# Kernel tuning notes

Hardware: AMD Instinct MI355X
Metric: run time of the kernel (lower is better)

## Reference

```python
import jax, jax.numpy as jnp
import numpy as np

N = 100000   # nodes
E = 400000   # edges (before self-loops)
G = 4000     # graphs in batch
F_IN = 32    # node_embedding
HID = 128    # hidden_channels
H = 3        # heads (hard-coded in module)
W3 = H * HID # 384, post-concat width
NC = 10      # num_classes
NL = 4       # num_layers
NEG_SLOPE = 0.2


def _lin(key, fan_in, fan_out):
    return jax.random.normal(key, (fan_in, fan_out), jnp.float32) * (1.0 / np.sqrt(fan_in))


def setup_inputs() -> dict:
    key = jax.random.key(0)
    ks = iter(jax.random.split(key, 40))
    x = jax.random.normal(next(ks), (N, F_IN), jnp.float32)
    edge_index = jax.random.randint(next(ks), (2, E), 0, N, dtype=jnp.int32)
    batch = jnp.sort(jax.random.randint(next(ks), (N,), 0, G, dtype=jnp.int32))
    inp = dict(x=x, edge_index=edge_index, batch=batch)
    # MLP stem
    inp['lin1_w'] = _lin(next(ks), F_IN, 2 * HID); inp['lin1_b'] = jnp.zeros((2 * HID,), jnp.float32)
    inp['lin2_w'] = _lin(next(ks), 2 * HID, HID);  inp['lin2_b'] = jnp.zeros((HID,), jnp.float32)
    # conv1: GATConv(HID -> HID, heads=3)
    inp['w0'] = _lin(next(ks), HID, W3)
    inp['as0'] = jax.random.normal(next(ks), (H, HID), jnp.float32) * 0.1
    inp['ad0'] = jax.random.normal(next(ks), (H, HID), jnp.float32) * 0.1
    inp['b0'] = jnp.zeros((W3,), jnp.float32)
    # remaining NL-1 convs: GATConv(W3 -> HID, heads=3), stacked
    inp['wl'] = jnp.stack([_lin(next(ks), W3, W3) for _ in range(NL - 1)])
    inp['asl'] = jax.random.normal(next(ks), (NL - 1, H, HID), jnp.float32) * 0.1
    inp['adl'] = jax.random.normal(next(ks), (NL - 1, H, HID), jnp.float32) * 0.1
    inp['bl'] = jnp.zeros((NL - 1, W3), jnp.float32)
    # batch norms (NL total, all width W3)
    inp['gamma'] = jnp.ones((NL, W3), jnp.float32)
    inp['beta'] = jnp.zeros((NL, W3), jnp.float32)
    # head
    inp['lin3_w'] = _lin(next(ks), W3, HID); inp['lin3_b'] = jnp.zeros((HID,), jnp.float32)
    inp['lin4_w'] = _lin(next(ks), HID, NC); inp['lin4_b'] = jnp.zeros((NC,), jnp.float32)
    return inp


def _gat(x, W, a_src, a_dst, bias, src, dst):
    # PyG GATConv, concat heads. x: [N, Fin]
    h = (x @ W).reshape(N, H, HID)                       # [N, H, C]
    es = jnp.einsum('nhc,hc->nh', h, a_src)              # [N, H]
    ed = jnp.einsum('nhc,hc->nh', h, a_dst)
    e = jax.nn.leaky_relu(es[src] + ed[dst], NEG_SLOPE)  # [Etot, H]
    m = jax.ops.segment_max(e, dst, num_segments=N)      # segment softmax over incoming edges
    p = jnp.exp(e - m[dst])
    s = jax.ops.segment_sum(p, dst, num_segments=N)
    alpha = p / s[dst]                                   # every node has a self-loop -> s>0
    out = jax.ops.segment_sum(alpha[:, :, None] * h[src], dst, num_segments=N)
    return out.reshape(N, W3) + bias


def _bn(x, g, b):
    mu = x.mean(0)
    var = x.var(0)
    return (x - mu) * jax.lax.rsqrt(var + 1e-5) * g + b


def reference(x, edge_index, batch, lin1_w, lin1_b, lin2_w, lin2_b,
              w0, as0, ad0, b0, wl, asl, adl, bl, gamma, beta,
              lin3_w, lin3_b, lin4_w, lin4_b):
    loop = jnp.arange(N, dtype=edge_index.dtype)
    src = jnp.concatenate([edge_index[0], loop])  # add_self_loops=True (PyG default)
    dst = jnp.concatenate([edge_index[1], loop])
    h = jax.nn.relu(x @ lin1_w + lin1_b)
    h = jax.nn.relu(h @ lin2_w + lin2_b)
    h = _gat(h, w0, as0, ad0, b0, src, dst)
    h = _bn(h, gamma[0], beta[0])
    for i in range(NL - 1):
        h = _gat(h, wl[i], asl[i], adl[i], bl[i], src, dst)
        h = _bn(h, gamma[i + 1], beta[i + 1])
    # global mean pool over graphs
    sums = jax.ops.segment_sum(h, batch, num_segments=G)
    cnt = jax.ops.segment_sum(jnp.ones((N,), h.dtype), batch, num_segments=G)
    g = sums / jnp.maximum(cnt, 1.0)[:, None]
    g = jax.nn.relu(g @ lin3_w + lin3_b)
    logits = g @ lin4_w + lin4_b
    return jax.nn.log_softmax(logits, axis=-1)
```

## Files before the change

### kernel.cpp

```cpp
#include <hip/hip_runtime.h>

#define NN      100000
#define NN2     100096
#define NE      400000
#define ETOT    500000
#define NG      4000
#define W3D     384
#define HIDD    128
#define NCLS    10
#define NSLICE  256

typedef unsigned short u16;
typedef unsigned int   u32;
typedef unsigned long long u64;
typedef __attribute__((ext_vector_type(8))) short short8;
typedef __attribute__((ext_vector_type(4))) float f32x4;

static __device__ __forceinline__ float bf2f(u16 u) {
  return __uint_as_float(((u32)u) << 16);
}
static __device__ __forceinline__ float bflo(u32 u) {
  return __uint_as_float(u << 16);
}
static __device__ __forceinline__ float bfhi(u32 u) {
  return __uint_as_float(u & 0xffff0000u);
}
static __device__ __forceinline__ u16 f2b(float f) {
  u32 u = __float_as_uint(f);
  u32 r = (u + 0x7fffu + ((u >> 16) & 1u)) >> 16;
  return (u16)r;
}

static __device__ __forceinline__ void llds16(const u16* g, u16* l) {
  __builtin_amdgcn_global_load_lds(
      (const __attribute__((address_space(1))) void*)(u64)(const void*)g,
      (__attribute__((address_space(3))) void*)(u64)(void*)l, 16, 0, 0);
}

#define WAITV0() asm volatile("s_waitcnt vmcnt(0)" ::: "memory")

__global__ void mg_zero_out(float* out, int n) {
  int i = blockIdx.x * 256 + threadIdx.x;
  if (i < n) out[i] = 0.f;
}

__global__ void mg_cvt_x(const float* __restrict__ x, u16* __restrict__ Xb) {
  int idx = blockIdx.x * 256 + threadIdx.x;
  if (idx >= NN2 * 64) return;
  int row = idx >> 6, col = idx & 63;
  Xb[idx] = (row < NN && col < 32) ? f2b(x[row * 32 + col]) : (u16)0;
}

__global__ void mg_transpose_pad(const float* __restrict__ in, u16* __restrict__ out,
                                 int K, int Nn, int Kpad) {
  int idx = blockIdx.x * 256 + threadIdx.x;
  if (idx >= Nn * Kpad) return;
  int n = idx / Kpad, kp = idx - n * Kpad;
  out[idx] = (kp < K) ? f2b(in[kp * Nn + n]) : (u16)0;
}

__global__ void mg_fold_w(const u16* __restrict__ Wt, const float* __restrict__ scale,
                          const float* __restrict__ shift, u16* __restrict__ Wp,
                          float* __restrict__ bp) {
  __shared__ float red[128];
  int j = blockIdx.x, t = threadIdx.x;
  const u16* src = Wt + (size_t)j * (W3D + 8);
  u16* dst = Wp + (size_t)j * (W3D + 8);
  float acc = 0.f;
  for (int kp = t; kp < W3D + 8; kp += 128) {
    int kt = (kp < W3D) ? kp : 0;
    float w = bf2f(src[kp]);
    dst[kp] = f2b(w * scale[kt]);
    acc += w * shift[kt];
  }
  red[t] = acc; __syncthreads();
  for (int off = 64; off; off >>= 1) {
    if (t < off) red[t] += red[t + off];
    __syncthreads();
  }
  if (t == 0) bp[j] = red[0];
}

__global__ void mg_edge_histo(const int* __restrict__ ei, int* __restrict__ deg) {
  int e = blockIdx.x * 256 + threadIdx.x;
  if (e >= ETOT) return;
  int d = (e < NE) ? ei[NE + e] : (e - NE);
  atomicAdd(&deg[d], 1);
}

__global__ void mg_scan1(const int* __restrict__ in, int* __restrict__ bsum, int n) {
  __shared__ int sd[256];
  int tid = threadIdx.x;
  int base = blockIdx.x * 1024 + tid * 4;
  int s = 0;
#pragma unroll
  for (int j = 0; j < 4; ++j) { int i = base + j; if (i < n) s += in[i]; }
  sd[tid] = s; __syncthreads();
  for (int off = 128; off > 0; off >>= 1) {
    if (tid < off) sd[tid] += sd[tid + off];
    __syncthreads();
  }
  if (tid == 0) bsum[blockIdx.x] = sd[0];
}

__global__ void mg_scan2(int* __restrict__ bsum, int nb) {
  __shared__ int sd[256];
  int tid = threadIdx.x;
  int v = (tid < nb) ? bsum[tid] : 0;
  sd[tid] = v; __syncthreads();
  for (int off = 1; off < 256; off <<= 1) {
    int t = (tid >= off) ? sd[tid - off] : 0;
    __syncthreads();
    sd[tid] += t;
    __syncthreads();
  }
  if (tid < nb) bsum[tid] = sd[tid] - v;
}

__global__ void mg_scan3(const int* __restrict__ in, const int* __restrict__ bexcl,
                         int* __restrict__ out, int n) {
  __shared__ int sd[256];
  int tid = threadIdx.x;
  int base = blockIdx.x * 1024 + tid * 4;
  int loc[4]; int s = 0;
#pragma unroll
  for (int j = 0; j < 4; ++j) { int i = base + j; loc[j] = (i < n) ? in[i] : 0; s += loc[j]; }
  sd[tid] = s; __syncthreads();
  for (int off = 1; off < 256; off <<= 1) {
    int t = (tid >= off) ? sd[tid - off] : 0;
    __syncthreads();
    sd[tid] += t;
    __syncthreads();
  }
  int run = sd[tid] - s + bexcl[blockIdx.x];
#pragma unroll
  for (int j = 0; j < 4; ++j) {
    int i = base + j;
    if (i < n) { out[i] = run; run += loc[j]; if (i == n - 1) out[n] = run; }
  }
}

__global__ void mg_edge_scatter(const int* __restrict__ ei, int* __restrict__ fill,
                                int* __restrict__ colsrc, int* __restrict__ dstc) {
  int e = blockIdx.x * 256 + threadIdx.x;
  if (e >= ETOT) return;
  int s, d;
  if (e < NE) { s = ei[e]; d = ei[NE + e]; } else { s = e - NE; d = s; }
  int pos = atomicAdd(&fill[d], 1);
  colsrc[pos] = s;
  dstc[pos] = d;
}

__global__ void mg_graph_ptr(const int* __restrict__ batch, int* __restrict__ gptr) {
  int g = blockIdx.x * 256 + threadIdx.x;
  if (g > NG) return;
  if (g == NG) { gptr[NG] = NN; return; }
  int lo = 0, hi = NN;
  while (lo < hi) { int mid = (lo + hi) >> 1; if (batch[mid] < g) lo = mid + 1; else hi = mid; }
  gptr[g] = lo;
}

__global__ __launch_bounds__(256) void mg_edge_p(
    const int* __restrict__ colsrc, const int* __restrict__ dstc,
    const float* __restrict__ es, const float* __restrict__ ed,
    float* __restrict__ pcsr) {
  int e = blockIdx.x * 256 + threadIdx.x;
  if (e >= ETOT) return;
  int s = colsrc[e], d = dstc[e];
  float4 a = *(const float4*)(es + 4 * s);
  float4 sd = *(const float4*)(es + 4 * d);
  float4 dd = *(const float4*)(ed + 4 * d);
  float4 p;
  {
    float ev = a.x + dd.x; ev = (ev > 0.f) ? ev : 0.2f * ev;
    float mv = sd.x + dd.x; mv = (mv > 0.f) ? mv : 0.2f * mv;
    p.x = __expf(ev - mv);
  }
  {
    float ev = a.y + dd.y; ev = (ev > 0.f) ? ev : 0.2f * ev;
    float mv = sd.y + dd.y; mv = (mv > 0.f) ? mv : 0.2f * mv;
    p.y = __expf(ev - mv);
  }
  {
    float ev = a.z + dd.z; ev = (ev > 0.f) ? ev : 0.2f * ev;
    float mv = sd.z + dd.z; mv = (mv > 0.f) ? mv : 0.2f * mv;
    p.z = __expf(ev - mv);
  }
  p.w = 0.f;
  *(float4*)(pcsr + (size_t)e * 4) = p;
}

#define CP 136

template<int K>
__global__ __launch_bounds__(512, 2) void mg_gemm(
    const u16* __restrict__ Ag, const u16* __restrict__ Bt,
    int MT, int Mstore, int Nn,
    u16* __restrict__ Cb, const float* __restrict__ bias, int relu,
    const float* __restrict__ asrc, const float* __restrict__ adst,
    float* __restrict__ aes, float* __restrict__ aed) {
  constexpr int KP = K + 8;
  constexpr int NITER = K / 32;
  constexpr int CSZ = (K == 384) ? 3 : ((K >= 128) ? 2 : 1);
  constexpr int CH = NITER / CSZ;
  static_assert(CH * CSZ == NITER && (CH & 1) == 0, "chunking");
  __shared__ u16 lds[128 * KP + 8 * 16 * CP];
  u16* Blds = lds;
  int tid = threadIdx.x;
  int lane = tid & 63, wv = tid >> 6;

  int gx = gridDim.x, gy = gridDim.y;
  int nwg = gx * gy;
  int lin = (int)blockIdx.y * gx + blockIdx.x;
  int q = nwg >> 3, r8 = nwg & 7;
  int xcd = lin & 7, sidx = lin >> 3;
  int nlin = (xcd < r8) ? (xcd * (q + 1) + sidx)
                        : (r8 * (q + 1) + (xcd - r8) * q + sidx);
  int mchunk = nlin / gy;
  int nidx = nlin - mchunk * gy;
  int n0 = nidx * 128;

  int lr = lane & 15, lq = lane >> 4;

  {
    const u16* Bg = Bt + (size_t)n0 * KP;
    constexpr int BBYTES = 128 * KP * 2;
    constexpr int FULL = BBYTES / 8192;
    constexpr int REMC = (BBYTES - FULL * 8192) / 16;
#pragma unroll
    for (int s = 0; s < FULL; ++s) {
      int off = s * 4096 + wv * 512 + lane * 8;
      llds16(Bg + off, Blds + off);
    }
    if (REMC > 0 && wv * 64 + lane < REMC) {
      int off = FULL * 4096 + wv * 512 + lane * 8;
      llds16(Bg + off, Blds + off);
    }
  }

  float bvv[8];
#pragma unroll
  for (int ni = 0; ni < 8; ++ni)
    bvv[ni] = bias ? bias[n0 + ni * 16 + lr] : 0.f;

  WAITV0();
  __syncthreads();

  u16* strip = lds + 128 * KP + wv * (16 * CP);

  int t0 = (int)(((long long)mchunk * MT) / gx);
  int t1 = (int)(((long long)(mchunk + 1) * MT) / gx);

  f32x4 acc[2][8];
  short8 bufE[2][CSZ], bufO[2][CSZ];

  auto loadCh = [&](short8 (&buf)[2][CSZ], int t, int ch) {
    const u16* Ar = Ag + (size_t)(t * 256 + wv * 32 + lr) * K + lq * 8 + ch * (CSZ * 32);
#pragma unroll
    for (int mi = 0; mi < 2; ++mi)
#pragma unroll
      for (int s = 0; s < CSZ; ++s)
        buf[mi][s] = *(const short8*)(Ar + (size_t)mi * 16 * K + s * 32);
  };
  auto compCh = [&](short8 (&buf)[2][CSZ], int ch) {
#pragma unroll
    for (int s = 0; s < CSZ; ++s) {
      int it = ch * CSZ + s;
      short8 bfr[8];
#pragma unroll
      for (int ni = 0; ni < 8; ++ni)
        bfr[ni] = *(const short8*)(Blds + (ni * 16 + lr) * KP + it * 32 + lq * 8);
#pragma unroll
      for (int mi = 0; mi < 2; ++mi)
#pragma unroll
        for (int ni = 0; ni < 8; ++ni)
          acc[mi][ni] = __builtin_amdgcn_mfma_f32_16x16x32_bf16(buf[mi][s], bfr[ni], acc[mi][ni], 0, 0, 0);
    }
  };

  loadCh(bufE, t0, 0);

  for (int t = t0; t < t1; ++t) {
    int rowbase = t * 256 + wv * 32;
#pragma unroll
    for (int mi = 0; mi < 2; ++mi)
#pragma unroll
      for (int ni = 0; ni < 8; ++ni) acc[mi][ni] = (f32x4){0.f, 0.f, 0.f, 0.f};

#pragma unroll
    for (int ch = 0; ch < CH; ch += 2) {
      loadCh(bufO, t, ch + 1);
      compCh(bufE, ch);
      if (ch + 2 < CH) loadCh(bufE, t, ch + 2);
      else if (t + 1 < t1) loadCh(bufE, t + 1, 0);
      compCh(bufO, ch + 1);
    }

#pragma unroll
    for (int mi = 0; mi < 2; ++mi) {
#pragma unroll
      for (int ni = 0; ni < 8; ++ni) {
#pragma unroll
        for (int r = 0; r < 4; ++r) {
          float v = acc[mi][ni][r] + bvv[ni];
          if (relu) v = fmaxf(v, 0.f);
          strip[(lq * 4 + r) * CP + ni * 16 + lr] = f2b(v);
        }
      }
      int row16 = lane >> 2, cb = lane & 3;
      const u16* src = strip + row16 * CP + cb * 32;
      uint4 c0 = *(const uint4*)(src);
      uint4 c1 = *(const uint4*)(src + 8);
      uint4 c2 = *(const uint4*)(src + 16);
      uint4 c3 = *(const uint4*)(src + 24);
      int mrow = rowbase + mi * 16 + row16;
      u16* gout = Cb + (size_t)mrow * Nn + n0 + cb * 32;
      *(uint4*)(gout)      = c0;
      *(uint4*)(gout + 8)  = c1;
      *(uint4*)(gout + 16) = c2;
      *(uint4*)(gout + 24) = c3;

      if (aes) {
        const float* ap = asrc + n0 + cb * 32;
        const float* dp = adst + n0 + cb * 32;
        float se = 0.f, de = 0.f;
        uint4 cj[4] = {c0, c1, c2, c3};
#pragma unroll
        for (int j = 0; j < 4; ++j) {
          float4 A0 = *(const float4*)(ap + j * 8);
          float4 A1 = *(const float4*)(ap + j * 8 + 4);
          float4 D0 = *(const float4*)(dp + j * 8);
          float4 D1 = *(const float4*)(dp + j * 8 + 4);
          uint4 rv = cj[j];
          float v0 = bflo(rv.x), v1 = bfhi(rv.x), v2 = bflo(rv.y), v3 = bfhi(rv.y);
          float v4 = bflo(rv.z), v5 = bfhi(rv.z), v6 = bflo(rv.w), v7 = bfhi(rv.w);
          se += v0 * A0.x + v1 * A0.y + v2 * A0.z + v3 * A0.w
              + v4 * A1.x + v5 * A1.y + v6 * A1.z + v7 * A1.w;
          de += v0 * D0.x + v1 * D0.y + v2 * D0.z + v3 * D0.w
              + v4 * D1.x + v5 * D1.y + v6 * D1.z + v7 * D1.w;
        }
        se += __shfl_xor(se, 1); se += __shfl_xor(se, 2);
        de += __shfl_xor(de, 1); de += __shfl_xor(de, 2);
        if (cb == 0 && mrow < Mstore) {
          aes[mrow * 4 + nidx] = se;
          aed[mrow * 4 + nidx] = de;
        }
      }
    }
  }
}

__global__ __launch_bounds__(256) void mg_aggregate(
    const u16* __restrict__ B, const float* __restrict__ pcsr,
    const int* __restrict__ rowptr, const int* __restrict__ colsrc,
    const float* __restrict__ bias,
    u16* __restrict__ A, float* __restrict__ stats) {
  __shared__ float bS[4 * W3D];
  __shared__ float bQ[4 * W3D];
  int wv = threadIdx.x >> 6, lane = threadIdx.x & 63;
  if (lane < 48) {
    int h = lane >> 4;
    int cc = lane * 8;
    float4 bv0 = *(const float4*)(bias + cc);
    float4 bv1 = *(const float4*)(bias + cc + 4);
    float stS[8], stQ[8];
#pragma unroll
    for (int j = 0; j < 8; ++j) { stS[j] = 0.f; stQ[j] = 0.f; }
#pragma unroll
    for (int sub = 0; sub < 2; ++sub) {
      int n = blockIdx.x * 8 + wv * 2 + sub;
      int r0 = rowptr[n], r1 = rowptr[n + 1];
      float accv[8];
#pragma unroll
      for (int j = 0; j < 8; ++j) accv[j] = 0.f;
      float ssum = 0.f;

      int   c0, c1, c2, c3, cb0, cb1, cb2, cb3;
      float p0, p1, p2, p3, pb0, pb1, pb2, pb3;
      uint4 v0, v1, v2, v3;

#define IDX_(CV, PV, RR) { int _i = ((RR) < r1) ? (RR) : (r1 - 1);          \
      CV = colsrc[_i]; PV = pcsr[(size_t)_i * 4 + h]; }
#define BLD_(VV, CV) { int _s = __builtin_amdgcn_readfirstlane(CV);         \
      VV = *(const uint4*)(B + (size_t)_s * W3D + cc); }
#define CMP_(PV, VV, RR) { float _pv = ((RR) < r1) ? PV : 0.f;              \
      ssum += _pv;                                                          \
      accv[0] += _pv * bflo(VV.x); accv[1] += _pv * bfhi(VV.x);             \
      accv[2] += _pv * bflo(VV.y); accv[3] += _pv * bfhi(VV.y);             \
      accv[4] += _pv * bflo(VV.z); accv[5] += _pv * bfhi(VV.z);             \
      accv[6] += _pv * bflo(VV.w); accv[7] += _pv * bfhi(VV.w); }

      IDX_(c0,  p0,  r0 + 0) IDX_(c1,  p1,  r0 + 1)
      IDX_(c2,  p2,  r0 + 2) IDX_(c3,  p3,  r0 + 3)
      IDX_(cb0, pb0, r0 + 4) IDX_(cb1, pb1, r0 + 5)
      IDX_(cb2, pb2, r0 + 6) IDX_(cb3, pb3, r0 + 7)
      BLD_(v0, c0) BLD_(v1, c1) BLD_(v2, c2) BLD_(v3, c3)

      for (int base = r0; base < r1; base += 4) {
        CMP_(p0, v0, base + 0)  BLD_(v0, cb0)
        CMP_(p1, v1, base + 1)  BLD_(v1, cb1)
        CMP_(p2, v2, base + 2)  BLD_(v2, cb2)
        CMP_(p3, v3, base + 3)  BLD_(v3, cb3)
        p0 = pb0; p1 = pb1; p2 = pb2; p3 = pb3;
        IDX_(cb0, pb0, base + 8)  IDX_(cb1, pb1, base + 9)
        IDX_(cb2, pb2, base + 10) IDX_(cb3, pb3, base + 11)
      }
#undef IDX_
#undef BLD_
#undef CMP_

      float inv = 1.0f / ssum;
      float v[8];
      v[0] = accv[0] * inv + bv0.x; v[1] = accv[1] * inv + bv0.y;
      v[2] = accv[2] * inv + bv0.z; v[3] = accv[3] * inv + bv0.w;
      v[4] = accv[4] * inv + bv1.x; v[5] = accv[5] * inv + bv1.y;
      v[6] = accv[6] * inv + bv1.z; v[7] = accv[7] * inv + bv1.w;
      uint4 st;
      st.x = (u32)f2b(v[0]) | ((u32)f2b(v[1]) << 16);
      st.y = (u32)f2b(v[2]) | ((u32)f2b(v[3]) << 16);
      st.z = (u32)f2b(v[4]) | ((u32)f2b(v[5]) << 16);
      st.w = (u32)f2b(v[6]) | ((u32)f2b(v[7]) << 16);
      *(uint4*)(A + (size_t)n * W3D + cc) = st;
#pragma unroll
      for (int j = 0; j < 8; ++j) { stS[j] += v[j]; stQ[j] += v[j] * v[j]; }
    }
    *(float4*)(bS + wv * W3D + cc)     = (float4){stS[0], stS[1], stS[2], stS[3]};
    *(float4*)(bS + wv * W3D + cc + 4) = (float4){stS[4], stS[5], stS[6], stS[7]};
    *(float4*)(bQ + wv * W3D + cc)     = (float4){stQ[0], stQ[1], stQ[2], stQ[3]};
    *(float4*)(bQ + wv * W3D + cc + 4) = (float4){stQ[4], stQ[5], stQ[6], stQ[7]};
  }
  __syncthreads();
  for (int t = threadIdx.x; t < W3D; t += 256) {
    float s = 0.f, q = 0.f;
#pragma unroll
    for (int w = 0; w < 4; ++w) { s += bS[w * W3D + t]; q += bQ[w * W3D + t]; }
    float* sl = stats + (size_t)(blockIdx.x & (NSLICE - 1)) * 768;
    atomicAdd(&sl[t], s);
    atomicAdd(&sl[W3D + t], q);
  }
}

__global__ void mg_bn_finalize(const float* __restrict__ stats, const float* __restrict__ gamma,
                               const float* __restrict__ beta, float* __restrict__ scale,
                               float* __restrict__ shift) {
  int c = threadIdx.x;
  float s = 0.f, q = 0.f;
  for (int b = 0; b < NSLICE; ++b) { s += stats[b * 768 + c]; q += stats[b * 768 + W3D + c]; }
  const float invN = 1.0f / (float)NN;
  float mu = s * invN;
  float var = fmaxf(q * invN - mu * mu, 0.f);
  float inv = rsqrtf(var + 1e-5f);
  float g = gamma[c], be = beta[c];
  scale[c] = g * inv;
  shift[c] = be - mu * g * inv;
}

__global__ void mg_pool(const u16* __restrict__ A, const float* __restrict__ scale,
                        const float* __restrict__ shift, const int* __restrict__ gptr,
                        float* __restrict__ pooled) {
  int g = blockIdx.x, c = threadIdx.x;
  int r0 = gptr[g], r1 = gptr[g + 1];
  float acc = 0.f;
  for (int n = r0; n < r1; ++n) acc += bf2f(A[(size_t)n * W3D + c]);
  int cnt = r1 - r0;
  float v = (cnt > 0) ? (acc / (float)cnt) * scale[c] + shift[c] : 0.f;
  pooled[g * W3D + c] = v;
}

__global__ void mg_head(const float* __restrict__ pooled, const float* __restrict__ w3,
                        const float* __restrict__ b3, const float* __restrict__ w4,
                        const float* __restrict__ b4, float* __restrict__ out) {
  __shared__ float p[W3D];
  __shared__ float g2[HIDD];
  __shared__ float lg[NCLS];
  int g = blockIdx.x, t = threadIdx.x;
  for (int i = t; i < W3D; i += 128) p[i] = pooled[g * W3D + i];
  __syncthreads();
  float acc = 0.f;
  for (int k = 0; k < W3D; ++k) acc += p[k] * w3[k * HIDD + t];
  g2[t] = fmaxf(acc + b3[t], 0.f);
  __syncthreads();
  if (t < NCLS) {
    float a = 0.f;
    for (int k = 0; k < HIDD; ++k) a += g2[k] * w4[k * NCLS + t];
    lg[t] = a + b4[t];
  }
  __syncthreads();
  if (t < NCLS) {
    float m = -1e30f;
#pragma unroll
    for (int j = 0; j < NCLS; ++j) m = fmaxf(m, lg[j]);
    float se = 0.f;
#pragma unroll
    for (int j = 0; j < NCLS; ++j) se += __expf(lg[j] - m);
    out[g * NCLS + t] = lg[t] - m - __logf(se);
  }
}

extern "C" void kernel_launch(void* const* d_in, const int* in_sizes, int n_in,
                              void* d_out, int out_size, void* d_ws, size_t ws_size,
                              hipStream_t stream) {
  const float* x     = (const float*)d_in[0];
  const int*   ei    = (const int*)d_in[1];
  const int*   batch = (const int*)d_in[2];
  const float* w1    = (const float*)d_in[3];
  const float* b1    = (const float*)d_in[4];
  const float* w2    = (const float*)d_in[5];
  const float* b2    = (const float*)d_in[6];
  const float* w0    = (const float*)d_in[7];
  const float* as0   = (const float*)d_in[8];
  const float* ad0   = (const float*)d_in[9];
  const float* b0    = (const float*)d_in[10];
  const float* wl    = (const float*)d_in[11];
  const float* asl   = (const float*)d_in[12];
  const float* adl   = (const float*)d_in[13];
  const float* bl    = (const float*)d_in[14];
  const float* gamma = (const float*)d_in[15];
  const float* beta  = (const float*)d_in[16];
  const float* w3    = (const float*)d_in[17];
  const float* b3    = (const float*)d_in[18];
  const float* w4    = (const float*)d_in[19];
  const float* b4    = (const float*)d_in[20];
  float* out = (float*)d_out;

  char* w = (char*)d_ws;
  auto alloc = [&](size_t bytes) -> void* {
    void* p = (void*)w;
    w += (bytes + 255) & ~(size_t)255;
    return p;
  };
  u16*   P      = (u16*)alloc((size_t)NN2 * W3D * 2);
  u16*   Q      = (u16*)alloc((size_t)NN2 * W3D * 2);
  float* es     = (float*)alloc((size_t)NN * 4 * 4);
  float* ed     = (float*)alloc((size_t)NN * 4 * 4);
  int*   deg    = (int*)alloc((size_t)NN * 4);
  int*   rowptr = (int*)alloc((size_t)(NN + 1) * 4);
  int*   fill   = (int*)alloc((size_t)NN * 4);
  int*   colsrc = (int*)alloc((size_t)ETOT * 4);
  int*   dstc   = (int*)alloc((size_t)ETOT * 4);
  float* pcsr   = (float*)alloc((size_t)ETOT * 4 * 4);
  int*   bsum   = (int*)alloc(256 * 4);
  float* stats  = (float*)alloc((size_t)NSLICE * 768 * 4);
  float* scale  = (float*)alloc(W3D * 4);
  float* shift  = (float*)alloc(W3D * 4);
  float* bprime = (float*)alloc(W3D * 4);
  int*   gptr   = (int*)alloc((size_t)(NG + 1) * 4);
  float* pooled = (float*)alloc((size_t)NG * W3D * 4);
  u16*   W1T    = (u16*)alloc((size_t)256 * 72 * 2);
  u16*   W2T    = (u16*)alloc((size_t)128 * 264 * 2);
  u16*   W0T    = (u16*)alloc((size_t)384 * 136 * 2);
  u16*   WlT    = (u16*)alloc((size_t)3 * 384 * 392 * 2);
  u16*   WpT    = (u16*)alloc((size_t)384 * 392 * 2);
  u16*   Xb     = Q;

  if ((size_t)(w - (char*)d_ws) > ws_size) {
    mg_zero_out<<<(out_size + 255) / 256, 256, 0, stream>>>(out, out_size);
    return;
  }

  mg_cvt_x<<<(NN2 * 64 + 255) / 256, 256, 0, stream>>>(x, Xb);
  mg_transpose_pad<<<(256 * 72 + 255) / 256, 256, 0, stream>>>(w1, W1T, 32, 256, 72);
  mg_transpose_pad<<<(128 * 264 + 255) / 256, 256, 0, stream>>>(w2, W2T, 256, 128, 264);
  mg_transpose_pad<<<(384 * 136 + 255) / 256, 256, 0, stream>>>(w0, W0T, 128, 384, 136);
  for (int i = 0; i < 3; ++i)
    mg_transpose_pad<<<(384 * 392 + 255) / 256, 256, 0, stream>>>(
        wl + (size_t)i * 384 * 384, WlT + (size_t)i * 384 * 392, 384, 384, 392);

  hipMemsetAsync(deg, 0, (size_t)NN * 4, stream);
  mg_edge_histo<<<(ETOT + 255) / 256, 256, 0, stream>>>(ei, deg);
  int nb = (NN + 1023) / 1024;
  mg_scan1<<<nb, 256, 0, stream>>>(deg, bsum, NN);
  mg_scan2<<<1, 256, 0, stream>>>(bsum, nb);
  mg_scan3<<<nb, 256, 0, stream>>>(deg, bsum, rowptr, NN);
  hipMemcpyAsync(fill, rowptr, (size_t)NN * 4, hipMemcpyDeviceToDevice, stream);
  mg_edge_scatter<<<(ETOT + 255) / 256, 256, 0, stream>>>(ei, fill, colsrc, dstc);
  mg_graph_ptr<<<(NG + 1 + 255) / 256, 256, 0, stream>>>(batch, gptr);

  dim3 blk(512);
  const int MT = NN2 / 256;
  const int EPB = (ETOT + 255) / 256;

  mg_gemm<64><<<dim3(128, 2), blk, 0, stream>>>(Xb, W1T, MT, NN, 256,
                                                P, b1, 1,
                                                nullptr, nullptr, nullptr, nullptr);
  mg_gemm<256><<<dim3(256, 1), blk, 0, stream>>>(P, W2T, MT, NN, 128,
                                                 Q, b2, 1,
                                                 nullptr, nullptr, nullptr, nullptr);

  for (int i = 0; i < 4; ++i) {
    const float* bi_g = nullptr;
    const u16* Bt;
    if (i == 0) {
      Bt = W0T;
    } else {
      mg_fold_w<<<384, 128, 0, stream>>>(WlT + (size_t)(i - 1) * 384 * 392,
                                         scale, shift, WpT, bprime);
      Bt = WpT;
      bi_g = bprime;
    }
    const float* as = (i == 0) ? as0 : (asl + (size_t)(i - 1) * 384);
    const float* ad = (i == 0) ? ad0 : (adl + (size_t)(i - 1) * 384);
    const float* bi = (i == 0) ? b0  : (bl  + (size_t)(i - 1) * 384);
    hipMemsetAsync(stats, 0, (size_t)NSLICE * 768 * 4, stream);
    if (i == 0)
      mg_gemm<128><<<dim3(85, 3), blk, 0, stream>>>(Q, Bt, MT, NN, W3D,
                                                    P, bi_g, 0,
                                                    as, ad, es, ed);
    else
      mg_gemm<384><<<dim3(85, 3), blk, 0, stream>>>(Q, Bt, MT, NN, W3D,
                                                    P, bi_g, 0,
                                                    as, ad, es, ed);
    mg_edge_p<<<EPB, 256, 0, stream>>>(colsrc, dstc, es, ed, pcsr);
    mg_aggregate<<<NN / 8, 256, 0, stream>>>(P, pcsr, rowptr, colsrc, bi, Q, stats);
    mg_bn_finalize<<<1, 384, 0, stream>>>(stats, gamma + (size_t)i * W3D,
                                          beta + (size_t)i * W3D, scale, shift);
  }

  mg_pool<<<NG, 384, 0, stream>>>(Q, scale, shift, gptr, pooled);
  mg_head<<<NG, 128, 0, stream>>>(pooled, w3, b3, w4, b4, out);
}
```

Before: 972.0 us.

## Halve GEMM N-tile to 64 columns and split attention logits into half-head partials

The GEMM now computes 64-column output tiles instead of 128. That halves the accumulators, the LDS B-tile and the strip buffer, so launch bounds can request 4 waves per SIMD and the grid doubles along N. Because each head (128 columns) now spans two tiles, the fused attention-score epilogue writes two partial dot products per head into 8-wide es/ed arrays. The edge kernel sums each pair when it reads them. The trade-off is more A-matrix reloads (each A row is read by twice as many workgroups), extra edge-kernel gather traffic, and padding NN2 to a larger multiple.

```diff
diff --git a/kernel.cpp b/kernel.cpp
--- a/kernel.cpp
+++ b/kernel.cpp
@@ -1,7 +1,7 @@
 #include <hip/hip_runtime.h>
 
 #define NN      100000
-#define NN2     100096
+#define NN2     100352
 #define NE      400000
 #define ETOT    500000
 #define NG      4000
@@ -162,38 +162,44 @@
 
 __global__ __launch_bounds__(256) void mg_edge_p(
     const int* __restrict__ colsrc, const int* __restrict__ dstc,
-    const float* __restrict__ es, const float* __restrict__ ed,
+    const float* __restrict__ es8, const float* __restrict__ ed8,
     float* __restrict__ pcsr) {
   int e = blockIdx.x * 256 + threadIdx.x;
   if (e >= ETOT) return;
   int s = colsrc[e], d = dstc[e];
-  float4 a = *(const float4*)(es + 4 * s);
-  float4 sd = *(const float4*)(es + 4 * d);
-  float4 dd = *(const float4*)(ed + 4 * d);
+  float4 sa0 = *(const float4*)(es8 + 8 * s);
+  float4 sa1 = *(const float4*)(es8 + 8 * s + 4);
+  float4 da0 = *(const float4*)(es8 + 8 * d);
+  float4 da1 = *(const float4*)(es8 + 8 * d + 4);
+  float4 dd0 = *(const float4*)(ed8 + 8 * d);
+  float4 dd1 = *(const float4*)(ed8 + 8 * d + 4);
+  float esx = sa0.x + sa0.y, esy = sa0.z + sa0.w, esz = sa1.x + sa1.y;
+  float sdx = da0.x + da0.y, sdy = da0.z + da0.w, sdz = da1.x + da1.y;
+  float ddx = dd0.x + dd0.y, ddy = dd0.z + dd0.w, ddz = dd1.x + dd1.y;
   float4 p;
   {
-    float ev = a.x + dd.x; ev = (ev > 0.f) ? ev : 0.2f * ev;
-    float mv = sd.x + dd.x; mv = (mv > 0.f) ? mv : 0.2f * mv;
+    float ev = esx + ddx; ev = (ev > 0.f) ? ev : 0.2f * ev;
+    float mv = sdx + ddx; mv = (mv > 0.f) ? mv : 0.2f * mv;
     p.x = __expf(ev - mv);
   }
   {
-    float ev = a.y + dd.y; ev = (ev > 0.f) ? ev : 0.2f * ev;
-    float mv = sd.y + dd.y; mv = (mv > 0.f) ? mv : 0.2f * mv;
+    float ev = esy + ddy; ev = (ev > 0.f) ? ev : 0.2f * ev;
+    float mv = sdy + ddy; mv = (mv > 0.f) ? mv : 0.2f * mv;
     p.y = __expf(ev - mv);
   }
   {
-    float ev = a.z + dd.z; ev = (ev > 0.f) ? ev : 0.2f * ev;
-    float mv = sd.z + dd.z; mv = (mv > 0.f) ? mv : 0.2f * mv;
+    float ev = esz + ddz; ev = (ev > 0.f) ? ev : 0.2f * ev;
+    float mv = sdz + ddz; mv = (mv > 0.f) ? mv : 0.2f * mv;
     p.z = __expf(ev - mv);
   }
   p.w = 0.f;
   *(float4*)(pcsr + (size_t)e * 4) = p;
 }
 
-#define CP 136
+#define CPN 72
 
 template<int K>
-__global__ __launch_bounds__(512, 2) void mg_gemm(
+__global__ __launch_bounds__(512, 4) void mg_gemm(
     const u16* __restrict__ Ag, const u16* __restrict__ Bt,
     int MT, int Mstore, int Nn,
     u16* __restrict__ Cb, const float* __restrict__ bias, int relu,
@@ -201,10 +207,10 @@
     float* __restrict__ aes, float* __restrict__ aed) {
   constexpr int KP = K + 8;
   constexpr int NITER = K / 32;
-  constexpr int CSZ = (K == 384) ? 3 : ((K >= 128) ? 2 : 1);
+  constexpr int CSZ = (K == 64) ? 1 : 2;
   constexpr int CH = NITER / CSZ;
   static_assert(CH * CSZ == NITER && (CH & 1) == 0, "chunking");
-  __shared__ u16 lds[128 * KP + 8 * 16 * CP];
+  __shared__ u16 lds[64 * KP + 8 * 16 * CPN];
   u16* Blds = lds;
   int tid = threadIdx.x;
   int lane = tid & 63, wv = tid >> 6;
@@ -218,13 +224,13 @@
                         : (r8 * (q + 1) + (xcd - r8) * q + sidx);
   int mchunk = nlin / gy;
   int nidx = nlin - mchunk * gy;
-  int n0 = nidx * 128;
+  int n0 = nidx * 64;
 
   int lr = lane & 15, lq = lane >> 4;
 
   {
     const u16* Bg = Bt + (size_t)n0 * KP;
-    constexpr int BBYTES = 128 * KP * 2;
+    constexpr int BBYTES = 64 * KP * 2;
     constexpr int FULL = BBYTES / 8192;
     constexpr int REMC = (BBYTES - FULL * 8192) / 16;
 #pragma unroll
@@ -238,20 +244,20 @@
     }
   }
 
-  float bvv[8];
-#pragma unroll
-  for (int ni = 0; ni < 8; ++ni)
+  float bvv[4];
+#pragma unroll
+  for (int ni = 0; ni < 4; ++ni)
     bvv[ni] = bias ? bias[n0 + ni * 16 + lr] : 0.f;
 
   WAITV0();
   __syncthreads();
 
-  u16* strip = lds + 128 * KP + wv * (16 * CP);
+  u16* strip = lds + 64 * KP + wv * (16 * CPN);
 
   int t0 = (int)(((long long)mchunk * MT) / gx);
   int t1 = (int)(((long long)(mchunk + 1) * MT) / gx);
 
-  f32x4 acc[2][8];
+  f32x4 acc[2][4];
   short8 bufE[2][CSZ], bufO[2][CSZ];
 
   auto loadCh = [&](short8 (&buf)[2][CSZ], int t, int ch) {
@@ -266,14 +272,14 @@
 #pragma unroll
     for (int s = 0; s < CSZ; ++s) {
       int it = ch * CSZ + s;
-      short8 bfr[8];
-#pragma unroll
-      for (int ni = 0; ni < 8; ++ni)
+      short8 bfr[4];
+#pragma unroll
+      for (int ni = 0; ni < 4; ++ni)
         bfr[ni] = *(const short8*)(Blds + (ni * 16 + lr) * KP + it * 32 + lq * 8);
 #pragma unroll
       for (int mi = 0; mi < 2; ++mi)
 #pragma unroll
-        for (int ni = 0; ni < 8; ++ni)
+        for (int ni = 0; ni < 4; ++ni)
           acc[mi][ni] = __builtin_amdgcn_mfma_f32_16x16x32_bf16(buf[mi][s], bfr[ni], acc[mi][ni], 0, 0, 0);
     }
   };
@@ -285,7 +291,7 @@
 #pragma unroll
     for (int mi = 0; mi < 2; ++mi)
 #pragma unroll
-      for (int ni = 0; ni < 8; ++ni) acc[mi][ni] = (f32x4){0.f, 0.f, 0.f, 0.f};
+      for (int ni = 0; ni < 4; ++ni) acc[mi][ni] = (f32x4){0.f, 0.f, 0.f, 0.f};
 
 #pragma unroll
     for (int ch = 0; ch < CH; ch += 2) {
@@ -299,51 +305,56 @@
 #pragma unroll
     for (int mi = 0; mi < 2; ++mi) {
 #pragma unroll
-      for (int ni = 0; ni < 8; ++ni) {
+      for (int ni = 0; ni < 4; ++ni) {
 #pragma unroll
         for (int r = 0; r < 4; ++r) {
           float v = acc[mi][ni][r] + bvv[ni];
           if (relu) v = fmaxf(v, 0.f);
-          strip[(lq * 4 + r) * CP + ni * 16 + lr] = f2b(v);
+          strip[(lq * 4 + r) * CPN + ni * 16 + lr] = f2b(v);
         }
       }
       int row16 = lane >> 2, cb = lane & 3;
-      const u16* src = strip + row16 * CP + cb * 32;
+      const u16* src = strip + row16 * CPN + cb * 16;
       uint4 c0 = *(const uint4*)(src);
       uint4 c1 = *(const uint4*)(src + 8);
-      uint4 c2 = *(const uint4*)(src + 16);
-      uint4 c3 = *(const uint4*)(src + 24);
       int mrow = rowbase + mi * 16 + row16;
-      u16* gout = Cb + (size_t)mrow * Nn + n0 + cb * 32;
-      *(uint4*)(gout)      = c0;
-      *(uint4*)(gout + 8)  = c1;
-      *(uint4*)(gout + 16) = c2;
-      *(uint4*)(gout + 24) = c3;
+      u16* gout = Cb + (size_t)mrow * Nn + n0 + cb * 16;
+      *(uint4*)(gout)     = c0;
+      *(uint4*)(gout + 8) = c1;
 
       if (aes) {
-        const float* ap = asrc + n0 + cb * 32;
-        const float* dp = adst + n0 + cb * 32;
-        float se = 0.f, de = 0.f;
-        uint4 cj[4] = {c0, c1, c2, c3};
-#pragma unroll
-        for (int j = 0; j < 4; ++j) {
-          float4 A0 = *(const float4*)(ap + j * 8);
-          float4 A1 = *(const float4*)(ap + j * 8 + 4);
-          float4 D0 = *(const float4*)(dp + j * 8);
-          float4 D1 = *(const float4*)(dp + j * 8 + 4);
-          uint4 rv = cj[j];
-          float v0 = bflo(rv.x), v1 = bfhi(rv.x), v2 = bflo(rv.y), v3 = bfhi(rv.y);
-          float v4 = bflo(rv.z), v5 = bfhi(rv.z), v6 = bflo(rv.w), v7 = bfhi(rv.w);
-          se += v0 * A0.x + v1 * A0.y + v2 * A0.z + v3 * A0.w
-              + v4 * A1.x + v5 * A1.y + v6 * A1.z + v7 * A1.w;
-          de += v0 * D0.x + v1 * D0.y + v2 * D0.z + v3 * D0.w
-              + v4 * D1.x + v5 * D1.y + v6 * D1.z + v7 * D1.w;
+        const float* ap = asrc + n0 + cb * 16;
+        const float* dp = adst + n0 + cb * 16;
+        float4 A0 = *(const float4*)(ap);
+        float4 A1 = *(const float4*)(ap + 4);
+        float4 A2 = *(const float4*)(ap + 8);
+        float4 A3 = *(const float4*)(ap + 12);
+        float4 D0 = *(const float4*)(dp);
+        float4 D1 = *(const float4*)(dp + 4);
+        float4 D2 = *(const float4*)(dp + 8);
+        float4 D3 = *(const float4*)(dp + 12);
+        float se, de;
+        {
+          float v0 = bflo(c0.x), v1 = bfhi(c0.x), v2 = bflo(c0.y), v3 = bfhi(c0.y);
+          float v4 = bflo(c0.z), v5 = bfhi(c0.z), v6 = bflo(c0.w), v7 = bfhi(c0.w);
+          se = v0 * A0.x + v1 * A0.y + v2 * A0.z + v3 * A0.w
+             + v4 * A1.x + v5 * A1.y + v6 * A1.z + v7 * A1.w;
+          de = v0 * D0.x + v1 * D0.y + v2 * D0.z + v3 * D0.w
+             + v4 * D1.x + v5 * D1.y + v6 * D1.z + v7 * D1.w;
+        }
+        {
+          float v0 = bflo(c1.x), v1 = bfhi(c1.x), v2 = bflo(c1.y), v3 = bfhi(c1.y);
+          float v4 = bflo(c1.z), v5 = bfhi(c1.z), v6 = bflo(c1.w), v7 = bfhi(c1.w);
+          se += v0 * A2.x + v1 * A2.y + v2 * A2.z + v3 * A2.w
+              + v4 * A3.x + v5 * A3.y + v6 * A3.z + v7 * A3.w;
+          de += v0 * D2.x + v1 * D2.y + v2 * D2.z + v3 * D2.w
+              + v4 * D3.x + v5 * D3.y + v6 * D3.z + v7 * D3.w;
         }
         se += __shfl_xor(se, 1); se += __shfl_xor(se, 2);
         de += __shfl_xor(de, 1); de += __shfl_xor(de, 2);
         if (cb == 0 && mrow < Mstore) {
-          aes[mrow * 4 + nidx] = se;
-          aed[mrow * 4 + nidx] = de;
+          aes[(size_t)mrow * 8 + nidx] = se;
+          aed[(size_t)mrow * 8 + nidx] = de;
         }
       }
     }
@@ -531,8 +542,8 @@
   };
   u16*   P      = (u16*)alloc((size_t)NN2 * W3D * 2);
   u16*   Q      = (u16*)alloc((size_t)NN2 * W3D * 2);
-  float* es     = (float*)alloc((size_t)NN * 4 * 4);
-  float* ed     = (float*)alloc((size_t)NN * 4 * 4);
+  float* es     = (float*)alloc((size_t)NN * 8 * 4);
+  float* ed     = (float*)alloc((size_t)NN * 8 * 4);
   int*   deg    = (int*)alloc((size_t)NN * 4);
   int*   rowptr = (int*)alloc((size_t)(NN + 1) * 4);
   int*   fill   = (int*)alloc((size_t)NN * 4);
@@ -580,10 +591,10 @@
   const int MT = NN2 / 256;
   const int EPB = (ETOT + 255) / 256;
 
-  mg_gemm<64><<<dim3(128, 2), blk, 0, stream>>>(Xb, W1T, MT, NN, 256,
+  mg_gemm<64><<<dim3(128, 4), blk, 0, stream>>>(Xb, W1T, MT, NN, 256,
                                                 P, b1, 1,
                                                 nullptr, nullptr, nullptr, nullptr);
-  mg_gemm<256><<<dim3(256, 1), blk, 0, stream>>>(P, W2T, MT, NN, 128,
+  mg_gemm<256><<<dim3(256, 2), blk, 0, stream>>>(P, W2T, MT, NN, 128,
                                                  Q, b2, 1,
                                                  nullptr, nullptr, nullptr, nullptr);
 
@@ -603,11 +614,11 @@
     const float* bi = (i == 0) ? b0  : (bl  + (size_t)(i - 1) * 384);
     hipMemsetAsync(stats, 0, (size_t)NSLICE * 768 * 4, stream);
     if (i == 0)
-      mg_gemm<128><<<dim3(85, 3), blk, 0, stream>>>(Q, Bt, MT, NN, W3D,
+      mg_gemm<128><<<dim3(85, 6), blk, 0, stream>>>(Q, Bt, MT, NN, W3D,
                                                     P, bi_g, 0,
                                                     as, ad, es, ed);
     else
-      mg_gemm<384><<<dim3(85, 3), blk, 0, stream>>>(Q, Bt, MT, NN, W3D,
+      mg_gemm<384><<<dim3(85, 6), blk, 0, stream>>>(Q, Bt, MT, NN, W3D,
                                                     P, bi_g, 0,
                                                     as, ad, es, ed);
     mg_edge_p<<<EPB, 256, 0, stream>>>(colsrc, dstc, es, ed, pcsr);
```

Measured after the change: 967.1 us. Within noise of the previous version (-0.5%).
